# Kernel tuning notes

Hardware: AMD Instinct MI355X
Metric: run time of the kernel (lower is better)

The kernel has to match this reference:

```python
import jax, jax.numpy as jnp
import numpy as np

N, D_IN, D_OUT = 16384, 64, 64
AVG_DEG = 32.0
L2_EPS = 1e-12  # torch F.normalize default eps


def setup_inputs() -> dict:
    key = jax.random.key(0)
    kx, ka, kw, kb = jax.random.split(key, 4)
    X = jax.random.normal(kx, (N, D_IN), dtype=jnp.float32)
    # binary adjacency with avg degree ~AVG_DEG (module treats adj as 0/1 mask)
    adj = (jax.random.uniform(ka, (N, N)) < (AVG_DEG / N)).astype(jnp.float32)
    # nn.Linear(2*D_IN, D_OUT): store W as (2*D_IN, D_OUT) for x @ W + b
    bound = 1.0 / np.sqrt(2 * D_IN)
    W = jax.random.uniform(kw, (2 * D_IN, D_OUT), dtype=jnp.float32, minval=-bound, maxval=bound)
    b = jax.random.uniform(kb, (D_OUT,), dtype=jnp.float32, minval=-bound, maxval=bound)
    return {"X": X, "adj": adj, "W": W, "b": b}


def reference(X, adj, W, b):
    # eval-mode mean aggregation: h_neigh = (adj + I) @ X / clamp(rowsum(adj + I), 1)
    # (adj + I) @ X == adj @ X + X, avoiding materializing the NxN identity.
    deg = jnp.clip(jnp.sum(adj, axis=1, keepdims=True) + 1.0, 1.0, None)  # (N,1)
    h_neigh = (adj @ X + X) / deg                                          # (N,D)
    concat = jnp.concatenate([X, h_neigh], axis=1)                         # (N,2D)
    z = concat @ W + b                                                     # (N,O)
    out = jax.nn.relu(z)
    norm = jnp.linalg.norm(out, axis=1, keepdims=True)
    return out / jnp.maximum(norm, L2_EPS)
```

## Files before the change

### kernel.cpp

```cpp
#include <hip/hip_runtime.h>
#include <stdint.h>


#define NROWS   16384
#define DDIM    64
#define MAXNNZ  256
#define NBLOCKS 2048
#define TOTAL_WAVES (NBLOCKS * 4)
#define ROWS_PER_WAVE (NROWS / TOTAL_WAVES)

typedef uint32_t u32x4 __attribute__((ext_vector_type(4)));

__global__ __launch_bounds__(256, 4) void sage_fused(
    const float* __restrict__ X,
    const float* __restrict__ adj,
    const float* __restrict__ W,
    const float* __restrict__ bias,
    float* __restrict__ out)
{
    __shared__ int   slist[4][MAXNNZ];
    __shared__ int   scnt[4];
    __shared__ float scat[4][2 * DDIM];

    const int tid  = threadIdx.x;
    const int lane = tid & 63;
    const int w    = tid >> 6;
    const int gw   = blockIdx.x * 4 + w;

    const float bv = bias[lane];

    for (int r = 0; r < ROWS_PER_WAVE; ++r) {
        const int row = gw + r * TOTAL_WAVES;

        if (lane == 0) scnt[w] = 0;
        __builtin_amdgcn_wave_barrier();

        const u32x4* rowp = reinterpret_cast<const u32x4*>(adj + (size_t)row * NROWS);
        u32x4 c[4], n[4];
#pragma unroll
        for (int q = 0; q < 4; ++q)
            c[q] = __builtin_nontemporal_load(&rowp[q * 64 + lane]);

#pragma unroll 1
        for (int s = 0; s < 16; ++s) {
            if (s < 15) {
#pragma unroll
                for (int q = 0; q < 4; ++q)
                    n[q] = __builtin_nontemporal_load(&rowp[(s + 1) * 256 + q * 64 + lane]);
            }
#pragma unroll
            for (int q = 0; q < 4; ++q) {
                const u32x4 vv = c[q];
                if (vv.x | vv.y | vv.z | vv.w) {
                    const int base = (s * 256 + q * 64 + lane) * 4;
                    const uint32_t w4[4] = { vv.x, vv.y, vv.z, vv.w };
#pragma unroll
                    for (int j = 0; j < 4; ++j) {
                        if (w4[j]) {
                            const int p = atomicAdd(&scnt[w], 1);
                            if (p < MAXNNZ) slist[w][p] = base + j;
                        }
                    }
                }
            }
#pragma unroll
            for (int q = 0; q < 4; ++q) c[q] = n[q];
        }
        __builtin_amdgcn_wave_barrier();

        const int nnz = scnt[w];
        const int cn  = (nnz < MAXNNZ) ? nnz : MAXNNZ;

        float acc = 0.0f;
        int k = 0;
        for (; k + 4 <= cn; k += 4) {
            const int j0 = slist[w][k], j1 = slist[w][k + 1];
            const int j2 = slist[w][k + 2], j3 = slist[w][k + 3];
            const float a0 = X[(size_t)j0 * DDIM + lane];
            const float a1 = X[(size_t)j1 * DDIM + lane];
            const float a2 = X[(size_t)j2 * DDIM + lane];
            const float a3 = X[(size_t)j3 * DDIM + lane];
            acc += (a0 + a1) + (a2 + a3);
        }
        for (; k < cn; ++k) acc += X[(size_t)slist[w][k] * DDIM + lane];

        const float xi = X[(size_t)row * DDIM + lane];
        const float h  = (acc + xi) / ((float)nnz + 1.0f);
        scat[w][lane]        = xi;
        scat[w][DDIM + lane] = h;
        __builtin_amdgcn_wave_barrier();

        float z0 = bv, z1 = 0.0f, z2 = 0.0f, z3 = 0.0f;
#pragma unroll 8
        for (int kk = 0; kk < 2 * DDIM; kk += 4) {
            z0 = fmaf(scat[w][kk + 0], W[(kk + 0) * DDIM + lane], z0);
            z1 = fmaf(scat[w][kk + 1], W[(kk + 1) * DDIM + lane], z1);
            z2 = fmaf(scat[w][kk + 2], W[(kk + 2) * DDIM + lane], z2);
            z3 = fmaf(scat[w][kk + 3], W[(kk + 3) * DDIM + lane], z3);
        }
        float z = (z0 + z1) + (z2 + z3);
        z = fmaxf(z, 0.0f);

        float s2 = z * z;
#pragma unroll
        for (int off = 32; off >= 1; off >>= 1) s2 += __shfl_xor(s2, off);
        const float inv = 1.0f / fmaxf(sqrtf(s2), 1e-12f);
        out[(size_t)row * DDIM + lane] = z * inv;
    }
}

extern "C" void kernel_launch(void* const* d_in, const int* in_sizes, int n_in,
                              void* d_out, int out_size, void* d_ws, size_t ws_size,
                              hipStream_t stream) {
    const float* X   = (const float*)d_in[0];
    const float* adj = (const float*)d_in[1];
    const float* W   = (const float*)d_in[2];
    const float* b   = (const float*)d_in[3];
    float* out = (float*)d_out;
    sage_fused<<<NBLOCKS, 256, 0, stream>>>(X, adj, W, b, out);
}
```

Baseline: 1.337 ms.

## Split adjacency scan into grid-wide streaming kernel with global row buckets

Replaces the fused per-wave row scan with three kernels: zeroing per-row counters, a flat grid-stride streaming scan of the whole 1 GiB adjacency that appends nonzero column indices into per-row global buckets via atomics, and a separate aggregation/linear/normalize kernel that reads the buckets. The aim is a fully coalesced, evenly spread stream over adj to get closer to peak HBM bandwidth than per-row waves do. The cost is global atomics, extra launches and a workspace round trip. Neighbor order within a bucket becomes nondeterministic, so float summation order may vary.

```diff
diff --git a/kernel.cpp b/kernel.cpp
--- a/kernel.cpp
+++ b/kernel.cpp
@@ -5,108 +5,105 @@
 #define NROWS   16384
 #define DDIM    64
 #define MAXNNZ  256
-#define NBLOCKS 2048
-#define TOTAL_WAVES (NBLOCKS * 4)
-#define ROWS_PER_WAVE (NROWS / TOTAL_WAVES)
+#define SCAN_BLOCKS 8192
+#define CHUNKS  ((size_t)NROWS * NROWS / 4)
 
 typedef uint32_t u32x4 __attribute__((ext_vector_type(4)));
 
-__global__ __launch_bounds__(256, 4) void sage_fused(
+__global__ __launch_bounds__(256) void zero_cnt(int* __restrict__ cnt) {
+    cnt[blockIdx.x * 256 + threadIdx.x] = 0;
+}
+
+__device__ __forceinline__ void process_chunk(u32x4 vv, size_t ci,
+                                              int* __restrict__ cnt,
+                                              int* __restrict__ bucket) {
+    if (vv.x | vv.y | vv.z | vv.w) {
+        const int e    = (int)(ci << 2);
+        const int row  = e >> 14;
+        const int cb   = e & 16383;
+        const int nz   = (vv.x ? 1 : 0) + (vv.y ? 1 : 0) + (vv.z ? 1 : 0) + (vv.w ? 1 : 0);
+        int p = atomicAdd(&cnt[row], nz);
+        int* bp = bucket + (size_t)row * MAXNNZ;
+        if (vv.x) { if (p < MAXNNZ) bp[p] = cb + 0; ++p; }
+        if (vv.y) { if (p < MAXNNZ) bp[p] = cb + 1; ++p; }
+        if (vv.z) { if (p < MAXNNZ) bp[p] = cb + 2; ++p; }
+        if (vv.w) { if (p < MAXNNZ) bp[p] = cb + 3; ++p; }
+    }
+}
+
+__global__ __launch_bounds__(256) void scan_adj(const float* __restrict__ adj,
+                                                int* __restrict__ cnt,
+                                                int* __restrict__ bucket) {
+    const size_t T   = (size_t)SCAN_BLOCKS * 256;
+    const size_t tid = (size_t)blockIdx.x * 256 + threadIdx.x;
+    const u32x4* p   = reinterpret_cast<const u32x4*>(adj);
+#pragma unroll 1
+    for (size_t base = tid; base < CHUNKS; base += 4 * T) {
+        const u32x4 c0 = __builtin_nontemporal_load(&p[base]);
+        const u32x4 c1 = __builtin_nontemporal_load(&p[base + T]);
+        const u32x4 c2 = __builtin_nontemporal_load(&p[base + 2 * T]);
+        const u32x4 c3 = __builtin_nontemporal_load(&p[base + 3 * T]);
+        process_chunk(c0, base,         cnt, bucket);
+        process_chunk(c1, base + T,     cnt, bucket);
+        process_chunk(c2, base + 2 * T, cnt, bucket);
+        process_chunk(c3, base + 3 * T, cnt, bucket);
+    }
+}
+
+__global__ __launch_bounds__(256, 4) void sage_agg(
     const float* __restrict__ X,
-    const float* __restrict__ adj,
+    const int*   __restrict__ cnt,
+    const int*   __restrict__ bucket,
     const float* __restrict__ W,
     const float* __restrict__ bias,
     float* __restrict__ out)
 {
-    __shared__ int   slist[4][MAXNNZ];
-    __shared__ int   scnt[4];
     __shared__ float scat[4][2 * DDIM];
 
     const int tid  = threadIdx.x;
     const int lane = tid & 63;
     const int w    = tid >> 6;
-    const int gw   = blockIdx.x * 4 + w;
+    const int row  = blockIdx.x * 4 + w;
 
-    const float bv = bias[lane];
+    const float bv  = bias[lane];
+    const int   nnz = cnt[row];
+    const int   cn  = (nnz < MAXNNZ) ? nnz : MAXNNZ;
+    const int*  bp  = bucket + (size_t)row * MAXNNZ;
 
-    for (int r = 0; r < ROWS_PER_WAVE; ++r) {
-        const int row = gw + r * TOTAL_WAVES;
+    float acc = 0.0f;
+    int k = 0;
+    for (; k + 4 <= cn; k += 4) {
+        const int j0 = bp[k], j1 = bp[k + 1], j2 = bp[k + 2], j3 = bp[k + 3];
+        const float a0 = X[(size_t)j0 * DDIM + lane];
+        const float a1 = X[(size_t)j1 * DDIM + lane];
+        const float a2 = X[(size_t)j2 * DDIM + lane];
+        const float a3 = X[(size_t)j3 * DDIM + lane];
+        acc += (a0 + a1) + (a2 + a3);
+    }
+    for (; k < cn; ++k) acc += X[(size_t)bp[k] * DDIM + lane];
 
-        if (lane == 0) scnt[w] = 0;
-        __builtin_amdgcn_wave_barrier();
+    const float xi = X[(size_t)row * DDIM + lane];
+    const float h  = (acc + xi) / ((float)nnz + 1.0f);
+    scat[w][lane]        = xi;
+    scat[w][DDIM + lane] = h;
+    __builtin_amdgcn_wave_barrier();
 
-        const u32x4* rowp = reinterpret_cast<const u32x4*>(adj + (size_t)row * NROWS);
-        u32x4 c[4], n[4];
+    float z0 = bv, z1 = 0.0f, z2 = 0.0f, z3 = 0.0f;
+#pragma unroll 8
+    for (int kk = 0; kk < 2 * DDIM; kk += 4) {
+        z0 = fmaf(scat[w][kk + 0], W[(kk + 0) * DDIM + lane], z0);
+        z1 = fmaf(scat[w][kk + 1], W[(kk + 1) * DDIM + lane], z1);
+        z2 = fmaf(scat[w][kk + 2], W[(kk + 2) * DDIM + lane], z2);
+        z3 = fmaf(scat[w][kk + 3], W[(kk + 3) * DDIM + lane], z3);
+    }
+    float z = (z0 + z1) + (z2 + z3);
+    z = fmaxf(z, 0.0f);
+
+    float s2 = z * z;
 #pragma unroll
-        for (int q = 0; q < 4; ++q)
-            c[q] = __builtin_nontemporal_load(&rowp[q * 64 + lane]);
-
-#pragma unroll 1
-        for (int s = 0; s < 16; ++s) {
-            if (s < 15) {
-#pragma unroll
-                for (int q = 0; q < 4; ++q)
-                    n[q] = __builtin_nontemporal_load(&rowp[(s + 1) * 256 + q * 64 + lane]);
-            }
-#pragma unroll
-            for (int q = 0; q < 4; ++q) {
-                const u32x4 vv = c[q];
-                if (vv.x | vv.y | vv.z | vv.w) {
-                    const int base = (s * 256 + q * 64 + lane) * 4;
-                    const uint32_t w4[4] = { vv.x, vv.y, vv.z, vv.w };
-#pragma unroll
-                    for (int j = 0; j < 4; ++j) {
-                        if (w4[j]) {
-                            const int p = atomicAdd(&scnt[w], 1);
-                            if (p < MAXNNZ) slist[w][p] = base + j;
-                        }
-                    }
-                }
-            }
-#pragma unroll
-            for (int q = 0; q < 4; ++q) c[q] = n[q];
-        }
-        __builtin_amdgcn_wave_barrier();
-
-        const int nnz = scnt[w];
-        const int cn  = (nnz < MAXNNZ) ? nnz : MAXNNZ;
-
-        float acc = 0.0f;
-        int k = 0;
-        for (; k + 4 <= cn; k += 4) {
-            const int j0 = slist[w][k], j1 = slist[w][k + 1];
-            const int j2 = slist[w][k + 2], j3 = slist[w][k + 3];
-            const float a0 = X[(size_t)j0 * DDIM + lane];
-            const float a1 = X[(size_t)j1 * DDIM + lane];
-            const float a2 = X[(size_t)j2 * DDIM + lane];
-            const float a3 = X[(size_t)j3 * DDIM + lane];
-            acc += (a0 + a1) + (a2 + a3);
-        }
-        for (; k < cn; ++k) acc += X[(size_t)slist[w][k] * DDIM + lane];
-
-        const float xi = X[(size_t)row * DDIM + lane];
-        const float h  = (acc + xi) / ((float)nnz + 1.0f);
-        scat[w][lane]        = xi;
-        scat[w][DDIM + lane] = h;
-        __builtin_amdgcn_wave_barrier();
-
-        float z0 = bv, z1 = 0.0f, z2 = 0.0f, z3 = 0.0f;
-#pragma unroll 8
-        for (int kk = 0; kk < 2 * DDIM; kk += 4) {
-            z0 = fmaf(scat[w][kk + 0], W[(kk + 0) * DDIM + lane], z0);
-            z1 = fmaf(scat[w][kk + 1], W[(kk + 1) * DDIM + lane], z1);
-            z2 = fmaf(scat[w][kk + 2], W[(kk + 2) * DDIM + lane], z2);
-            z3 = fmaf(scat[w][kk + 3], W[(kk + 3) * DDIM + lane], z3);
-        }
-        float z = (z0 + z1) + (z2 + z3);
-        z = fmaxf(z, 0.0f);
-
-        float s2 = z * z;
-#pragma unroll
-        for (int off = 32; off >= 1; off >>= 1) s2 += __shfl_xor(s2, off);
-        const float inv = 1.0f / fmaxf(sqrtf(s2), 1e-12f);
-        out[(size_t)row * DDIM + lane] = z * inv;
-    }
+    for (int off = 32; off >= 1; off >>= 1) s2 += __shfl_xor(s2, off);
+    const float inv = 1.0f / fmaxf(sqrtf(s2), 1e-12f);
+    out[(size_t)row * DDIM + lane] = z * inv;
 }
 
 extern "C" void kernel_launch(void* const* d_in, const int* in_sizes, int n_in,
@@ -117,5 +114,11 @@
     const float* W   = (const float*)d_in[2];
     const float* b   = (const float*)d_in[3];
     float* out = (float*)d_out;
-    sage_fused<<<NBLOCKS, 256, 0, stream>>>(X, adj, W, b, out);
+
+    int* cnt    = (int*)d_ws;
+    int* bucket = (int*)((char*)d_ws + (64 << 10));
+
+    zero_cnt<<<NROWS / 256, 256, 0, stream>>>(cnt);
+    scan_adj<<<SCAN_BLOCKS, 256, 0, stream>>>(adj, cnt, bucket);
+    sage_agg<<<NROWS / 4, 256, 0, stream>>>(X, cnt, bucket, W, b, out);
 }
```

After: 1.380 ms. +3.2%, slower.

## Use one row per wave with deeper rotated adjacency prefetch

Applied to the files above, without the earlier changes.

Launches 4096 blocks so that each wave handles exactly one row, removing the per-wave row loop. The adjacency row is streamed with an 8-deep register prefetch pipeline instead of a 4-load double buffer. Each wave starts its scan at a row-dependent rotated offset so concurrent waves spread their accesses across memory channels. It also switches from nontemporal loads to ordinary loads. Together these aim to keep more memory requests in flight on the 1 GiB dense adjacency stream, which dominates the cost. The trade-offs are higher register pressure and a neighbour-list order that changes the float summation order.

```diff
diff --git a/kernel.cpp b/kernel.cpp
--- a/kernel.cpp
+++ b/kernel.cpp
@@ -5,9 +5,8 @@
 #define NROWS   16384
 #define DDIM    64
 #define MAXNNZ  256
-#define NBLOCKS 2048
-#define TOTAL_WAVES (NBLOCKS * 4)
-#define ROWS_PER_WAVE (NROWS / TOTAL_WAVES)
+#define NBLOCKS 4096
+#define PIPE    8
 
 typedef uint32_t u32x4 __attribute__((ext_vector_type(4)));
 
@@ -25,88 +24,85 @@
     const int tid  = threadIdx.x;
     const int lane = tid & 63;
     const int w    = tid >> 6;
-    const int gw   = blockIdx.x * 4 + w;
+    const int row  = blockIdx.x * 4 + w;
 
     const float bv = bias[lane];
 
-    for (int r = 0; r < ROWS_PER_WAVE; ++r) {
-        const int row = gw + r * TOTAL_WAVES;
+    if (lane == 0) scnt[w] = 0;
+    __builtin_amdgcn_wave_barrier();
 
-        if (lane == 0) scnt[w] = 0;
-        __builtin_amdgcn_wave_barrier();
+    const int start = (row * 37 + (row >> 6) * 13) & 63;
+    const u32x4* rowp = reinterpret_cast<const u32x4*>(adj + (size_t)row * NROWS);
 
-        const u32x4* rowp = reinterpret_cast<const u32x4*>(adj + (size_t)row * NROWS);
-        u32x4 c[4], n[4];
+    u32x4 buf[PIPE];
 #pragma unroll
-        for (int q = 0; q < 4; ++q)
-            c[q] = __builtin_nontemporal_load(&rowp[q * 64 + lane]);
+    for (int i = 0; i < PIPE; ++i)
+        buf[i] = rowp[((start + i) & 63) * 64 + lane];
 
 #pragma unroll 1
-        for (int s = 0; s < 16; ++s) {
-            if (s < 15) {
+    for (int so = 0; so < 64; so += PIPE) {
 #pragma unroll
-                for (int q = 0; q < 4; ++q)
-                    n[q] = __builtin_nontemporal_load(&rowp[(s + 1) * 256 + q * 64 + lane]);
-            }
+        for (int i = 0; i < PIPE; ++i) {
+            const int s  = so + i;
+            const int ss = (start + s) & 63;
+            const u32x4 vv = buf[i];
+            if (vv.x | vv.y | vv.z | vv.w) {
+                const int base = (ss * 64 + lane) * 4;
+                const uint32_t w4[4] = { vv.x, vv.y, vv.z, vv.w };
 #pragma unroll
-            for (int q = 0; q < 4; ++q) {
-                const u32x4 vv = c[q];
-                if (vv.x | vv.y | vv.z | vv.w) {
-                    const int base = (s * 256 + q * 64 + lane) * 4;
-                    const uint32_t w4[4] = { vv.x, vv.y, vv.z, vv.w };
-#pragma unroll
-                    for (int j = 0; j < 4; ++j) {
-                        if (w4[j]) {
-                            const int p = atomicAdd(&scnt[w], 1);
-                            if (p < MAXNNZ) slist[w][p] = base + j;
-                        }
+                for (int j = 0; j < 4; ++j) {
+                    if (w4[j]) {
+                        const int p = atomicAdd(&scnt[w], 1);
+                        if (p < MAXNNZ) slist[w][p] = base + j;
                     }
                 }
             }
+            if (so + PIPE < 64) {
+                const int sn = (start + s + PIPE) & 63;
+                buf[i] = rowp[sn * 64 + lane];
+            }
+        }
+    }
+    __builtin_amdgcn_wave_barrier();
+
+    const int nnz = scnt[w];
+    const int cn  = (nnz < MAXNNZ) ? nnz : MAXNNZ;
+
+    float acc = 0.0f;
+    int k = 0;
+    for (; k + 4 <= cn; k += 4) {
+        const int j0 = slist[w][k], j1 = slist[w][k + 1];
+        const int j2 = slist[w][k + 2], j3 = slist[w][k + 3];
+        const float a0 = X[(size_t)j0 * DDIM + lane];
+        const float a1 = X[(size_t)j1 * DDIM + lane];
+        const float a2 = X[(size_t)j2 * DDIM + lane];
+        const float a3 = X[(size_t)j3 * DDIM + lane];
+        acc += (a0 + a1) + (a2 + a3);
+    }
+    for (; k < cn; ++k) acc += X[(size_t)slist[w][k] * DDIM + lane];
+
+    const float xi = X[(size_t)row * DDIM + lane];
+    const float h  = (acc + xi) / ((float)nnz + 1.0f);
+    scat[w][lane]        = xi;
+    scat[w][DDIM + lane] = h;
+    __builtin_amdgcn_wave_barrier();
+
+    float z0 = bv, z1 = 0.0f, z2 = 0.0f, z3 = 0.0f;
+#pragma unroll 8
+    for (int kk = 0; kk < 2 * DDIM; kk += 4) {
+        z0 = fmaf(scat[w][kk + 0], W[(kk + 0) * DDIM + lane], z0);
+        z1 = fmaf(scat[w][kk + 1], W[(kk + 1) * DDIM + lane], z1);
+        z2 = fmaf(scat[w][kk + 2], W[(kk + 2) * DDIM + lane], z2);
+        z3 = fmaf(scat[w][kk + 3], W[(kk + 3) * DDIM + lane], z3);
+    }
+    float z = (z0 + z1) + (z2 + z3);
+    z = fmaxf(z, 0.0f);
+
+    float s2 = z * z;
 #pragma unroll
-            for (int q = 0; q < 4; ++q) c[q] = n[q];
-        }
-        __builtin_amdgcn_wave_barrier();
-
-        const int nnz = scnt[w];
-        const int cn  = (nnz < MAXNNZ) ? nnz : MAXNNZ;
-
-        float acc = 0.0f;
-        int k = 0;
-        for (; k + 4 <= cn; k += 4) {
-            const int j0 = slist[w][k], j1 = slist[w][k + 1];
-            const int j2 = slist[w][k + 2], j3 = slist[w][k + 3];
-            const float a0 = X[(size_t)j0 * DDIM + lane];
-            const float a1 = X[(size_t)j1 * DDIM + lane];
-            const float a2 = X[(size_t)j2 * DDIM + lane];
-            const float a3 = X[(size_t)j3 * DDIM + lane];
-            acc += (a0 + a1) + (a2 + a3);
-        }
-        for (; k < cn; ++k) acc += X[(size_t)slist[w][k] * DDIM + lane];
-
-        const float xi = X[(size_t)row * DDIM + lane];
-        const float h  = (acc + xi) / ((float)nnz + 1.0f);
-        scat[w][lane]        = xi;
-        scat[w][DDIM + lane] = h;
-        __builtin_amdgcn_wave_barrier();
-
-        float z0 = bv, z1 = 0.0f, z2 = 0.0f, z3 = 0.0f;
-#pragma unroll 8
-        for (int kk = 0; kk < 2 * DDIM; kk += 4) {
-            z0 = fmaf(scat[w][kk + 0], W[(kk + 0) * DDIM + lane], z0);
-            z1 = fmaf(scat[w][kk + 1], W[(kk + 1) * DDIM + lane], z1);
-            z2 = fmaf(scat[w][kk + 2], W[(kk + 2) * DDIM + lane], z2);
-            z3 = fmaf(scat[w][kk + 3], W[(kk + 3) * DDIM + lane], z3);
-        }
-        float z = (z0 + z1) + (z2 + z3);
-        z = fmaxf(z, 0.0f);
-
-        float s2 = z * z;
-#pragma unroll
-        for (int off = 32; off >= 1; off >>= 1) s2 += __shfl_xor(s2, off);
-        const float inv = 1.0f / fmaxf(sqrtf(s2), 1e-12f);
-        out[(size_t)row * DDIM + lane] = z * inv;
-    }
+    for (int off = 32; off >= 1; off >>= 1) s2 += __shfl_xor(s2, off);
+    const float inv = 1.0f / fmaxf(sqrtf(s2), 1e-12f);
+    out[(size_t)row * DDIM + lane] = z * inv;
 }
 
 extern "C" void kernel_launch(void* const* d_in, const int* in_sizes, int n_in,
```

Measured after the change: 1.334 ms. Within noise of the previous version (-0.2%).
